# Optimization experiments

Measured on AMD Instinct MI355X. Metric: run time of the kernel, lower is better.

## Reference

```python
import jax, jax.numpy as jnp
import numpy as np

C = 0.11512925464970229  # ln(10)/20
K = 15
FD = 128
FS = 160
OV = 40
MAX_LAG = 256
PAD_L = K // 2
PAD_R = K - 1 - PAD_L
LOG_GAIN_LIMIT = 10 * C
GAIN_A = (6.0 * C - (-6.0 * C)) / 2
GAIN_B = (6.0 * C + (-6.0 * C)) / 2


def setup_inputs() -> dict:
    key = jax.random.key(0)
    ks = jax.random.split(key, 8)
    B, NF = 32, 500
    N = NF * FS
    x = jax.random.normal(ks[0], (B, 1, N), dtype=jnp.float32)
    features = jax.random.normal(ks[1], (B, NF, FD), dtype=jnp.float32)
    lags = jax.random.randint(ks[2], (B, NF), 0, 256)
    s = 1.0 / np.sqrt(FD)
    ck_w = jax.random.normal(ks[3], (K, FD), dtype=jnp.float32) * s
    ck_b = jax.random.normal(ks[4], (K,), dtype=jnp.float32) * 0.01
    fg_w = jax.random.normal(ks[5], (1, FD), dtype=jnp.float32) * s
    fg_b = jnp.full((1,), max(0.1, 4.0 + LOG_GAIN_LIMIT), dtype=jnp.float32)
    gg_w = jax.random.normal(ks[6], (1, FD), dtype=jnp.float32) * s
    gg_b = jax.random.normal(ks[7], (1,), dtype=jnp.float32) * 0.01
    return {"x": x, "features": features, "lags": lags,
            "ck_w": ck_w, "ck_b": ck_b, "fg_w": fg_w, "fg_b": fg_b,
            "gg_w": gg_w, "gg_b": gg_b}


def reference(x, features, lags, ck_w, ck_b, fg_w, fg_b, gg_w, gg_b):
    B, _, N = x.shape
    NF = features.shape[1]
    OUT = FS + OV  # per-frame output length before crossfade

    # per-frame FIR kernels, p=2 normalized over taps
    kernels = jnp.einsum('bfd,kd->bfk', features, ck_w) + ck_b          # (B,NF,K)
    kernels = kernels / (1e-6 + jnp.sqrt(jnp.sum(kernels**2, -1, keepdims=True)))
    # per-frame scalar gains
    gains = jnp.exp(-jax.nn.relu(features @ fg_w[0] + fg_b[0]) + LOG_GAIN_LIMIT)   # (B,NF)
    ggains = jnp.exp(GAIN_A * jnp.tanh(features @ gg_w[0] + gg_b[0]) + GAIN_B)     # (B,NF)

    # pad: [PAD_L,PAD_R] for conv, then [MAX_LAG, OV] for lag gather / final frame
    xp = jnp.pad(x[:, 0, :], ((0, 0), (MAX_LAG + PAD_L, PAD_R + OV)))   # (B,Np)

    L = FS + K - 1 + OV
    t = jnp.arange(L)
    f_off = jnp.arange(NF) * FS
    cidx = t[None, None, :] + f_off[None, :, None] + MAX_LAG - lags[:, :, None]  # (B,NF,L)
    xx = xp[jnp.arange(B)[:, None, None], cidx]                         # (B,NF,L)

    # grouped conv1d == cross-correlation with per-frame kernel
    win = jnp.stack([xx[:, :, k:k + OUT] for k in range(K)], axis=-1)   # (B,NF,OUT,K)
    conv = jnp.einsum('bflk,bfk->bfl', win, kernels)                    # (B,NF,OUT)

    # dry path
    offset = MAX_LAG + PAD_L
    pt_idx = offset + f_off[:, None] + jnp.arange(OUT)[None, :]         # (NF,OUT)
    pt = xp[:, pt_idx]                                                  # (B,NF,OUT)

    new_chunk = ggains[:, :, None] * (conv * gains[:, :, None] + pt)    # (B,NF,OUT)

    # overlap-add crossfade between consecutive frames
    win2 = 0.5 + 0.5 * jnp.cos((jnp.arange(OV) + 0.5) * jnp.pi / OV)
    win1 = win2[::-1]
    tails = new_chunk[:, :, FS:]                                        # (B,NF,OV)
    prev = jnp.concatenate([jnp.zeros_like(tails[:, :1]), tails[:, :-1]], axis=1)
    head = new_chunk[:, :, :OV] * win1 + prev * win2
    out = jnp.concatenate([head, new_chunk[:, :, OV:FS]], axis=-1)      # (B,NF,FS)
    return out.reshape(B, 1, NF * FS)
```

## Files before the change

### kernel.cpp

```cpp
#include <hip/hip_runtime.h>
#include <math.h>

namespace {
constexpr int K = 15;
constexpr int FD = 128;
constexpr int FS = 160;
constexpr int OV = 40;
constexpr int NFRAMES = 500;
constexpr int NSAMP = NFRAMES * FS;
constexpr float C_CONST = 0.11512925464970229f;
constexpr float LOG_GAIN_LIMIT = 10.0f * C_CONST;
constexpr float GAIN_A = 6.0f * C_CONST;
constexpr float PI_F = 3.14159265358979323846f;

constexpr int K1FPB = 15;
constexpr int SFSTR = 132;
constexpr int GPF = FS / 4;
}

__global__ __launch_bounds__(256)
void params_kernel(const float* __restrict__ feat,
                   const float* __restrict__ ck_w,
                   const float* __restrict__ ck_b,
                   const float* __restrict__ fg_w,
                   const float* __restrict__ fg_b,
                   const float* __restrict__ gg_w,
                   const float* __restrict__ gg_b,
                   float* __restrict__ params,
                   int G)
{
    const int tid = threadIdx.x;
    const int g0  = blockIdx.x * K1FPB;

    __shared__ __align__(16) float sfeat[K1FPB][SFSTR];
    __shared__ float sdots[K1FPB][17];

    for (int i = tid; i < K1FPB * (FD / 4); i += 256) {
        const int fi = i >> 5;
        const int e4 = i & 31;
        const int g  = g0 + fi;
        float4 v = make_float4(0.f, 0.f, 0.f, 0.f);
        if (g < G) v = ((const float4*)feat)[(size_t)g * (FD / 4) + e4];
        *(float4*)&sfeat[fi][e4 * 4] = v;
    }
    __syncthreads();

    if (tid < K1FPB * 17) {
        const int fi = tid / 17;
        const int j  = tid - fi * 17;
        const float* wrow = (j < K) ? (ck_w + (size_t)j * FD)
                                    : ((j == K) ? fg_w : gg_w);
        const float4* w4 = (const float4*)wrow;
        const float4* f4 = (const float4*)&sfeat[fi][0];
        float4 acc = make_float4(0.f, 0.f, 0.f, 0.f);
        #pragma unroll
        for (int i = 0; i < FD / 4; ++i) {
            const float4 a = f4[i];
            const float4 w = w4[i];
            acc.x += a.x * w.x; acc.y += a.y * w.y;
            acc.z += a.z * w.z; acc.w += a.w * w.w;
        }
        const float bias = (j < K) ? ck_b[j] : ((j == K) ? fg_b[0] : gg_b[0]);
        sdots[fi][j] = acc.x + acc.y + acc.z + acc.w + bias;
    }
    __syncthreads();

    if (tid < K1FPB) {
        const int g = g0 + tid;
        if (g < G) {
            float kern[K];
            float n2 = 0.f;
            #pragma unroll
            for (int k = 0; k < K; ++k) {
                kern[k] = sdots[tid][k];
                n2 += kern[k] * kern[k];
            }
            const float inv   = 1.f / (1e-6f + sqrtf(n2));
            const float gain  = expf(-fmaxf(sdots[tid][K], 0.f) + LOG_GAIN_LIMIT);
            const float ggain = expf(GAIN_A * tanhf(sdots[tid][K + 1]));
            const float ks    = ggain * gain * inv;
            float p[16];
            #pragma unroll
            for (int k = 0; k < K; ++k) p[k] = ks * kern[k];
            p[15] = ggain;
            float4* dst = (float4*)(params + (size_t)g * 16);
            dst[0] = *(float4*)&p[0];
            dst[1] = *(float4*)&p[4];
            dst[2] = *(float4*)&p[8];
            dst[3] = *(float4*)&p[12];
        }
    }
}

__global__ __launch_bounds__(256)
void synth_kernel(const float* __restrict__ x,
                  const int*   __restrict__ lags,
                  const float* __restrict__ params,
                  float* __restrict__ out,
                  int total)
{
    const int gidx = blockIdx.x * 256 + threadIdx.x;
    if (gidx >= total) return;
    const int b  = gidx / (NFRAMES * GPF);
    const int r  = gidx - b * (NFRAMES * GPF);
    const int f  = r / GPF;
    const int gi = r - f * GPF;
    const int t  = gi * 4;

    const float* xb = x + (size_t)b * NSAMP;

    float w[20];
    {
        const int base = f * FS - lags[b * NFRAMES + f] - 7 + t;
        if (base >= 0 && base + 19 < NSAMP) {
            #pragma unroll
            for (int q = 0; q < 5; ++q)
                *(float4*)&w[4 * q] = *(const float4*)(xb + base + 4 * q);
        } else {
            #pragma unroll
            for (int j = 0; j < 20; ++j) {
                const int idx = base + j;
                w[j] = (idx >= 0 && idx < NSAMP) ? xb[idx] : 0.f;
            }
        }
    }

    float kc[16];
    {
        const float4* pp = (const float4*)(params + ((size_t)b * NFRAMES + f) * 16);
        #pragma unroll
        for (int q = 0; q < 4; ++q) *(float4*)&kc[4 * q] = pp[q];
    }

    const float4 pt = *(const float4*)(xb + f * FS + t);

    float4 res;
    {
        float c0 = 0.f, c1 = 0.f, c2 = 0.f, c3 = 0.f;
        #pragma unroll
        for (int k = 0; k < K; ++k) {
            const float kk = kc[k];
            c0 += w[k]     * kk;
            c1 += w[k + 1] * kk;
            c2 += w[k + 2] * kk;
            c3 += w[k + 3] * kk;
        }
        const float ps = kc[15];
        res.x = c0 + ps * pt.x; res.y = c1 + ps * pt.y;
        res.z = c2 + ps * pt.z; res.w = c3 + ps * pt.w;
    }

    if (gi < OV / 4) {
        float4 w2;
        w2.x = 0.5f + 0.5f * cosf(((float)t + 0.5f) * (PI_F / OV));
        w2.y = 0.5f + 0.5f * cosf(((float)t + 1.5f) * (PI_F / OV));
        w2.z = 0.5f + 0.5f * cosf(((float)t + 2.5f) * (PI_F / OV));
        w2.w = 0.5f + 0.5f * cosf(((float)t + 3.5f) * (PI_F / OV));
        if (f > 0) {
            float wv[20];
            const int base2 = (f - 1) * FS - lags[b * NFRAMES + f - 1] - 7 + FS + t;
            if (base2 >= 0 && base2 + 19 < NSAMP) {
                #pragma unroll
                for (int q = 0; q < 5; ++q)
                    *(float4*)&wv[4 * q] = *(const float4*)(xb + base2 + 4 * q);
            } else {
                #pragma unroll
                for (int j = 0; j < 20; ++j) {
                    const int idx = base2 + j;
                    wv[j] = (idx >= 0 && idx < NSAMP) ? xb[idx] : 0.f;
                }
            }
            float qc[16];
            const float4* qq = (const float4*)(params + ((size_t)b * NFRAMES + f - 1) * 16);
            #pragma unroll
            for (int q = 0; q < 4; ++q) *(float4*)&qc[4 * q] = qq[q];

            float c0 = 0.f, c1 = 0.f, c2 = 0.f, c3 = 0.f;
            #pragma unroll
            for (int k = 0; k < K; ++k) {
                const float kk = qc[k];
                c0 += wv[k]     * kk;
                c1 += wv[k + 1] * kk;
                c2 += wv[k + 2] * kk;
                c3 += wv[k + 3] * kk;
            }
            const float ps = qc[15];
            const float4 tail = make_float4(c0 + ps * pt.x, c1 + ps * pt.y,
                                            c2 + ps * pt.z, c3 + ps * pt.w);
            res.x = res.x * (1.f - w2.x) + tail.x * w2.x;
            res.y = res.y * (1.f - w2.y) + tail.y * w2.y;
            res.z = res.z * (1.f - w2.z) + tail.z * w2.z;
            res.w = res.w * (1.f - w2.w) + tail.w * w2.w;
        } else {
            res.x *= (1.f - w2.x); res.y *= (1.f - w2.y);
            res.z *= (1.f - w2.z); res.w *= (1.f - w2.w);
        }
    }

    *(float4*)(out + (size_t)b * NSAMP + f * FS + t) = res;
}

extern "C" void kernel_launch(void* const* d_in, const int* in_sizes, int n_in,
                              void* d_out, int out_size, void* d_ws, size_t ws_size,
                              hipStream_t stream) {
    const float* x    = (const float*)d_in[0];
    const float* feat = (const float*)d_in[1];
    const int*   lags = (const int*)d_in[2];
    const float* ck_w = (const float*)d_in[3];
    const float* ck_b = (const float*)d_in[4];
    const float* fg_w = (const float*)d_in[5];
    const float* fg_b = (const float*)d_in[6];
    const float* gg_w = (const float*)d_in[7];
    const float* gg_b = (const float*)d_in[8];
    float* out    = (float*)d_out;
    float* params = (float*)d_ws;

    const int B = in_sizes[0] / NSAMP;
    const int G = B * NFRAMES;

    const int nblk1 = (G + K1FPB - 1) / K1FPB;
    params_kernel<<<dim3(nblk1), dim3(256), 0, stream>>>(
        feat, ck_w, ck_b, fg_w, fg_b, gg_w, gg_b, params, G);

    const int total = G * GPF;
    const int nblk2 = (total + 255) / 256;
    synth_kernel<<<dim3(nblk2), dim3(256), 0, stream>>>(
        x, lags, params, out, total);
}
```

Before: 111.0 us.

## Fuse parameter and synthesis kernels into one block-per-frame-group kernel

```diff
diff --git a/kernel.cpp b/kernel.cpp
--- a/kernel.cpp
+++ b/kernel.cpp
@@ -13,45 +13,55 @@
 constexpr float GAIN_A = 6.0f * C_CONST;
 constexpr float PI_F = 3.14159265358979323846f;
 
-constexpr int K1FPB = 15;
+constexpr int FPB = 6;
+constexpr int NFR = FPB + 1;
+constexpr int BPB = (NFRAMES + FPB - 1) / FPB;
 constexpr int SFSTR = 132;
 constexpr int GPF = FS / 4;
 }
 
 __global__ __launch_bounds__(256)
-void params_kernel(const float* __restrict__ feat,
-                   const float* __restrict__ ck_w,
-                   const float* __restrict__ ck_b,
-                   const float* __restrict__ fg_w,
-                   const float* __restrict__ fg_b,
-                   const float* __restrict__ gg_w,
-                   const float* __restrict__ gg_b,
-                   float* __restrict__ params,
-                   int G)
+void comb_fused(const float* __restrict__ x,
+                const float* __restrict__ feat,
+                const int*   __restrict__ lags,
+                const float* __restrict__ ck_w,
+                const float* __restrict__ ck_b,
+                const float* __restrict__ fg_w,
+                const float* __restrict__ fg_b,
+                const float* __restrict__ gg_w,
+                const float* __restrict__ gg_b,
+                float* __restrict__ out)
 {
     const int tid = threadIdx.x;
-    const int g0  = blockIdx.x * K1FPB;
-
-    __shared__ __align__(16) float sfeat[K1FPB][SFSTR];
-    __shared__ float sdots[K1FPB][17];
-
-    for (int i = tid; i < K1FPB * (FD / 4); i += 256) {
-        const int fi = i >> 5;
-        const int e4 = i & 31;
-        const int g  = g0 + fi;
+    const int bid = blockIdx.x;
+    const int b   = bid / BPB;
+    const int blk = bid - b * BPB;
+    const int f0  = blk * FPB;
+
+    __shared__ __align__(16) float sfeat[NFR][SFSTR];
+    __shared__ float sdots[NFR][17];
+    __shared__ __align__(16) float sfk[NFR][16];
+
+    const float* xb = x + (size_t)b * NSAMP;
+
+    if (tid < NFR * (FD / 4)) {
+        const int fr = tid >> 5;
+        const int e4 = tid & 31;
+        const int pf = f0 - 1 + fr;
         float4 v = make_float4(0.f, 0.f, 0.f, 0.f);
-        if (g < G) v = ((const float4*)feat)[(size_t)g * (FD / 4) + e4];
-        *(float4*)&sfeat[fi][e4 * 4] = v;
+        if (pf >= 0 && pf < NFRAMES)
+            v = ((const float4*)feat)[((size_t)b * NFRAMES + pf) * (FD / 4) + e4];
+        *(float4*)&sfeat[fr][e4 * 4] = v;
     }
     __syncthreads();
 
-    if (tid < K1FPB * 17) {
-        const int fi = tid / 17;
-        const int j  = tid - fi * 17;
+    if (tid < NFR * 17) {
+        const int fr = tid / 17;
+        const int j  = tid - fr * 17;
         const float* wrow = (j < K) ? (ck_w + (size_t)j * FD)
                                     : ((j == K) ? fg_w : gg_w);
         const float4* w4 = (const float4*)wrow;
-        const float4* f4 = (const float4*)&sfeat[fi][0];
+        const float4* f4 = (const float4*)&sfeat[fr][0];
         float4 acc = make_float4(0.f, 0.f, 0.f, 0.f);
         #pragma unroll
         for (int i = 0; i < FD / 4; ++i) {
@@ -61,13 +71,16 @@
             acc.z += a.z * w.z; acc.w += a.w * w.w;
         }
         const float bias = (j < K) ? ck_b[j] : ((j == K) ? fg_b[0] : gg_b[0]);
-        sdots[fi][j] = acc.x + acc.y + acc.z + acc.w + bias;
+        sdots[fr][j] = acc.x + acc.y + acc.z + acc.w + bias;
     }
     __syncthreads();
 
-    if (tid < K1FPB) {
-        const int g = g0 + tid;
-        if (g < G) {
+    if (tid < NFR) {
+        const int pf = f0 - 1 + tid;
+        if (pf < 0 || pf >= NFRAMES) {
+            #pragma unroll
+            for (int k = 0; k < 16; ++k) sfk[tid][k] = 0.f;
+        } else {
             float kern[K];
             float n2 = 0.f;
             #pragma unroll
@@ -79,125 +92,109 @@
             const float gain  = expf(-fmaxf(sdots[tid][K], 0.f) + LOG_GAIN_LIMIT);
             const float ggain = expf(GAIN_A * tanhf(sdots[tid][K + 1]));
             const float ks    = ggain * gain * inv;
-            float p[16];
-            #pragma unroll
-            for (int k = 0; k < K; ++k) p[k] = ks * kern[k];
-            p[15] = ggain;
-            float4* dst = (float4*)(params + (size_t)g * 16);
-            dst[0] = *(float4*)&p[0];
-            dst[1] = *(float4*)&p[4];
-            dst[2] = *(float4*)&p[8];
-            dst[3] = *(float4*)&p[12];
+            #pragma unroll
+            for (int k = 0; k < K; ++k) sfk[tid][k] = ks * kern[k];
+            sfk[tid][15] = ggain;
         }
     }
-}
-
-__global__ __launch_bounds__(256)
-void synth_kernel(const float* __restrict__ x,
-                  const int*   __restrict__ lags,
-                  const float* __restrict__ params,
-                  float* __restrict__ out,
-                  int total)
-{
-    const int gidx = blockIdx.x * 256 + threadIdx.x;
-    if (gidx >= total) return;
-    const int b  = gidx / (NFRAMES * GPF);
-    const int r  = gidx - b * (NFRAMES * GPF);
-    const int f  = r / GPF;
-    const int gi = r - f * GPF;
-    const int t  = gi * 4;
-
-    const float* xb = x + (size_t)b * NSAMP;
-
-    float w[20];
-    {
-        const int base = f * FS - lags[b * NFRAMES + f] - 7 + t;
-        if (base >= 0 && base + 19 < NSAMP) {
-            #pragma unroll
-            for (int q = 0; q < 5; ++q)
-                *(float4*)&w[4 * q] = *(const float4*)(xb + base + 4 * q);
-        } else {
-            #pragma unroll
-            for (int j = 0; j < 20; ++j) {
-                const int idx = base + j;
-                w[j] = (idx >= 0 && idx < NSAMP) ? xb[idx] : 0.f;
-            }
+    __syncthreads();
+
+    if (tid < FPB * GPF) {
+        const int frl = tid / GPF;
+        const int gi  = tid - frl * GPF;
+        const int t   = gi * 4;
+        const int f   = f0 + frl;
+        if (f < NFRAMES) {
+            const int fr = frl + 1;
+
+            float w[20];
+            {
+                const int base = f * FS - lags[b * NFRAMES + f] - 7 + t;
+                if (base >= 0 && base + 19 < NSAMP) {
+                    #pragma unroll
+                    for (int q = 0; q < 5; ++q)
+                        *(float4*)&w[4 * q] = *(const float4*)(xb + base + 4 * q);
+                } else {
+                    #pragma unroll
+                    for (int j = 0; j < 20; ++j) {
+                        const int idx = base + j;
+                        w[j] = (idx >= 0 && idx < NSAMP) ? xb[idx] : 0.f;
+                    }
+                }
+            }
+
+            float kc[16];
+            #pragma unroll
+            for (int q = 0; q < 4; ++q)
+                *(float4*)&kc[4 * q] = *(const float4*)&sfk[fr][4 * q];
+
+            const float4 pt = *(const float4*)(xb + f * FS + t);
+
+            float4 res;
+            {
+                float c0 = 0.f, c1 = 0.f, c2 = 0.f, c3 = 0.f;
+                #pragma unroll
+                for (int k = 0; k < K; ++k) {
+                    const float kk = kc[k];
+                    c0 += w[k]     * kk;
+                    c1 += w[k + 1] * kk;
+                    c2 += w[k + 2] * kk;
+                    c3 += w[k + 3] * kk;
+                }
+                const float ps = kc[15];
+                res.x = c0 + ps * pt.x; res.y = c1 + ps * pt.y;
+                res.z = c2 + ps * pt.z; res.w = c3 + ps * pt.w;
+            }
+
+            if (gi < OV / 4) {
+                float4 w2;
+                w2.x = 0.5f + 0.5f * cosf(((float)t + 0.5f) * (PI_F / OV));
+                w2.y = 0.5f + 0.5f * cosf(((float)t + 1.5f) * (PI_F / OV));
+                w2.z = 0.5f + 0.5f * cosf(((float)t + 2.5f) * (PI_F / OV));
+                w2.w = 0.5f + 0.5f * cosf(((float)t + 3.5f) * (PI_F / OV));
+
+                float4 tail = make_float4(0.f, 0.f, 0.f, 0.f);
+                if (f > 0) {
+                    float wv[20];
+                    const int base2 = (f - 1) * FS - lags[b * NFRAMES + f - 1] - 7 + FS + t;
+                    if (base2 >= 0 && base2 + 19 < NSAMP) {
+                        #pragma unroll
+                        for (int q = 0; q < 5; ++q)
+                            *(float4*)&wv[4 * q] = *(const float4*)(xb + base2 + 4 * q);
+                    } else {
+                        #pragma unroll
+                        for (int j = 0; j < 20; ++j) {
+                            const int idx = base2 + j;
+                            wv[j] = (idx >= 0 && idx < NSAMP) ? xb[idx] : 0.f;
+                        }
+                    }
+                    float qc[16];
+                    #pragma unroll
+                    for (int q = 0; q < 4; ++q)
+                        *(float4*)&qc[4 * q] = *(const float4*)&sfk[fr - 1][4 * q];
+
+                    float c0 = 0.f, c1 = 0.f, c2 = 0.f, c3 = 0.f;
+                    #pragma unroll
+                    for (int k = 0; k < K; ++k) {
+                        const float kk = qc[k];
+                        c0 += wv[k]     * kk;
+                        c1 += wv[k + 1] * kk;
+                        c2 += wv[k + 2] * kk;
+                        c3 += wv[k + 3] * kk;
+                    }
+                    const float ps = qc[15];
+                    tail = make_float4(c0 + ps * pt.x, c1 + ps * pt.y,
+                                       c2 + ps * pt.z, c3 + ps * pt.w);
+                }
+                res.x = res.x * (1.f - w2.x) + tail.x * w2.x;
+                res.y = res.y * (1.f - w2.y) + tail.y * w2.y;
+                res.z = res.z * (1.f - w2.z) + tail.z * w2.z;
+                res.w = res.w * (1.f - w2.w) + tail.w * w2.w;
+            }
+
+            *(float4*)(out + (size_t)b * NSAMP + f * FS + t) = res;
         }
     }
-
-    float kc[16];
-    {
-        const float4* pp = (const float4*)(params + ((size_t)b * NFRAMES + f) * 16);
-        #pragma unroll
-        for (int q = 0; q < 4; ++q) *(float4*)&kc[4 * q] = pp[q];
-    }
-
-    const float4 pt = *(const float4*)(xb + f * FS + t);
-
-    float4 res;
-    {
-        float c0 = 0.f, c1 = 0.f, c2 = 0.f, c3 = 0.f;
-        #pragma unroll
-        for (int k = 0; k < K; ++k) {
-            const float kk = kc[k];
-            c0 += w[k]     * kk;
-            c1 += w[k + 1] * kk;
-            c2 += w[k + 2] * kk;
-            c3 += w[k + 3] * kk;
-        }
-        const float ps = kc[15];
-        res.x = c0 + ps * pt.x; res.y = c1 + ps * pt.y;
-        res.z = c2 + ps * pt.z; res.w = c3 + ps * pt.w;
-    }
-
-    if (gi < OV / 4) {
-        float4 w2;
-        w2.x = 0.5f + 0.5f * cosf(((float)t + 0.5f) * (PI_F / OV));
-        w2.y = 0.5f + 0.5f * cosf(((float)t + 1.5f) * (PI_F / OV));
-        w2.z = 0.5f + 0.5f * cosf(((float)t + 2.5f) * (PI_F / OV));
-        w2.w = 0.5f + 0.5f * cosf(((float)t + 3.5f) * (PI_F / OV));
-        if (f > 0) {
-            float wv[20];
-            const int base2 = (f - 1) * FS - lags[b * NFRAMES + f - 1] - 7 + FS + t;
-            if (base2 >= 0 && base2 + 19 < NSAMP) {
-                #pragma unroll
-                for (int q = 0; q < 5; ++q)
-                    *(float4*)&wv[4 * q] = *(const float4*)(xb + base2 + 4 * q);
-            } else {
-                #pragma unroll
-                for (int j = 0; j < 20; ++j) {
-                    const int idx = base2 + j;
-                    wv[j] = (idx >= 0 && idx < NSAMP) ? xb[idx] : 0.f;
-                }
-            }
-            float qc[16];
-            const float4* qq = (const float4*)(params + ((size_t)b * NFRAMES + f - 1) * 16);
-            #pragma unroll
-            for (int q = 0; q < 4; ++q) *(float4*)&qc[4 * q] = qq[q];
-
-            float c0 = 0.f, c1 = 0.f, c2 = 0.f, c3 = 0.f;
-            #pragma unroll
-            for (int k = 0; k < K; ++k) {
-                const float kk = qc[k];
-                c0 += wv[k]     * kk;
-                c1 += wv[k + 1] * kk;
-                c2 += wv[k + 2] * kk;
-                c3 += wv[k + 3] * kk;
-            }
-            const float ps = qc[15];
-            const float4 tail = make_float4(c0 + ps * pt.x, c1 + ps * pt.y,
-                                            c2 + ps * pt.z, c3 + ps * pt.w);
-            res.x = res.x * (1.f - w2.x) + tail.x * w2.x;
-            res.y = res.y * (1.f - w2.y) + tail.y * w2.y;
-            res.z = res.z * (1.f - w2.z) + tail.z * w2.z;
-            res.w = res.w * (1.f - w2.w) + tail.w * w2.w;
-        } else {
-            res.x *= (1.f - w2.x); res.y *= (1.f - w2.y);
-            res.z *= (1.f - w2.z); res.w *= (1.f - w2.w);
-        }
-    }
-
-    *(float4*)(out + (size_t)b * NSAMP + f * FS + t) = res;
 }
 
 extern "C" void kernel_launch(void* const* d_in, const int* in_sizes, int n_in,
@@ -212,18 +209,9 @@
     const float* fg_b = (const float*)d_in[6];
     const float* gg_w = (const float*)d_in[7];
     const float* gg_b = (const float*)d_in[8];
-    float* out    = (float*)d_out;
-    float* params = (float*)d_ws;
+    float* out = (float*)d_out;
 
     const int B = in_sizes[0] / NSAMP;
-    const int G = B * NFRAMES;
-
-    const int nblk1 = (G + K1FPB - 1) / K1FPB;
-    params_kernel<<<dim3(nblk1), dim3(256), 0, stream>>>(
-        feat, ck_w, ck_b, fg_w, fg_b, gg_w, gg_b, params, G);
-
-    const int total = G * GPF;
-    const int nblk2 = (total + 255) / 256;
-    synth_kernel<<<dim3(nblk2), dim3(256), 0, stream>>>(
-        x, lags, params, out, total);
+    comb_fused<<<dim3(B * BPB), dim3(256), 0, stream>>>(
+        x, feat, lags, ck_w, ck_b, fg_w, fg_b, gg_w, gg_b, out);
 }
```

Measured after the change: 109.7 us. About the same (-1.1%).
